# Performance work log

Measured on AMD Instinct MI355X. Metric: run time of the kernel, lower is better.

Reference implementation:

```python
import jax, jax.numpy as jnp
import numpy as np

B, N, C, F = 8, 3, 64, 128
H = W = 128


def _up2(x):
    # nearest-neighbor upsample by 2 on the last two axes
    return jnp.repeat(jnp.repeat(x, 2, axis=-2), 2, axis=-1)


def setup_inputs() -> dict:
    key = jax.random.key(0)
    ks = jax.random.split(key, 12)
    s = lambda k, shp, fan: jax.random.normal(k, shp, jnp.float32) * (1.0 / np.sqrt(fan))
    return {
        "contexts": jax.random.normal(ks[0], (B, N, C, H, W), jnp.float32),
        "mainstream": jax.random.normal(ks[1], (B, F, H // 2, W // 2), jnp.float32),
        "Wc": s(ks[2], (C, C), C),        # W_context 1x1 conv weight [out,in]
        "bc": jnp.zeros((C,), jnp.float32),
        "Wf": s(ks[3], (C, F), F),        # W_feat 1x1
        "bf": jnp.zeros((C,), jnp.float32),
        "Wk": s(ks[4], (C, F), F),        # W_key_feat 1x1
        "bk": jnp.zeros((C,), jnp.float32),
        "Vw": s(ks[5], (C, F, 3, 3), F * 9),  # values_conv 3x3, OIHW
        "Vb": jnp.zeros((C,), jnp.float32),
    }


def reference(contexts, mainstream, Wc, bc, Wf, bf, Wk, bk, Vw, Vb):
    # contexts: [B,N,C,H,W], mainstream: [B,F,h,w]
    bias = lambda b: b[None, :, None, None]
    queries = jnp.einsum('bfhw,cf->bchw', mainstream, Wf) + bias(bf)       # [B,C,h,w]
    keys_m = jnp.einsum('bfhw,cf->bchw', mainstream, Wk) + bias(bk)        # [B,C,h,w]
    values = jax.lax.conv_general_dilated(
        mainstream, Vw, (1, 1), 'SAME',
        dimension_numbers=('NCHW', 'OIHW', 'NCHW')) + bias(Vb)             # [B,C,h,w]

    # stack contexts with upsampled mainstream keys, project with W_context (1x1)
    keys_stack = jnp.concatenate([contexts, _up2(keys_m)[:, None]], axis=1)  # [B,N+1,C,H,W]
    keys_proj = jnp.einsum('bnchw,dc->bndhw', keys_stack, Wc) + bc[None, None, :, None, None]

    q_up = _up2(queries)                                                    # [B,C,H,W]
    logits = jnp.einsum('bnchw,bchw->bnhw', keys_proj, q_up)                # [B,N+1,H,W]
    attn = jax.nn.softmax(logits, axis=1)                                   # softmax over contexts

    vals_stack = jnp.concatenate([contexts, _up2(values)[:, None]], axis=1) # [B,N+1,C,H,W]
    out = jnp.einsum('bnchw,bnhw->bchw', vals_stack, attn)                  # [B,C,H,W]
    return out
```

## Files before the change

kernel.cpp:

```cpp
#include <hip/hip_runtime.h>
#include <math.h>

#define CH   64
#define FD   128
#define HS   64
#define FS   128
#define NB   8
#define NCTX 3

#define WS_QT   0
#define WS_VAL  2097152
#define WS_L3   4194304
#define WS_BQ   4227072
#define WS_AVH  4227136
#define WS_AVL  4264000
#define WS_AQH  4300864
#define WS_AQL  4304960
#define WS_AKH  4309056
#define WS_AKL  4313152
#define WS_MTH  4317248
#define WS_MTL  6547520

typedef short  s16x8  __attribute__((ext_vector_type(8)));
typedef float  f32x16 __attribute__((ext_vector_type(16)));

__device__ inline unsigned short bf16_rne(float x) {
  unsigned u = __float_as_uint(x);
  u += 0x7FFFu + ((u >> 16) & 1u);
  return (unsigned short)(u >> 16);
}
__device__ inline void split2(float x, unsigned short& h, unsigned short& l) {
  h = bf16_rne(x);
  l = bf16_rne(x - __uint_as_float((unsigned)h << 16));
}

__global__ __launch_bounds__(256) void a_prep(
    const float* __restrict__ Wc, const float* __restrict__ Wf,
    const float* __restrict__ bf, const float* __restrict__ Wk,
    const float* __restrict__ Vw, float* __restrict__ ws) {
  int id = blockIdx.x * 256 + threadIdx.x;
  unsigned short* avh = (unsigned short*)(ws + WS_AVH);
  unsigned short* avl = (unsigned short*)(ws + WS_AVL);
  unsigned short* aqh = (unsigned short*)(ws + WS_AQH);
  unsigned short* aql = (unsigned short*)(ws + WS_AQL);
  unsigned short* akh = (unsigned short*)(ws + WS_AKH);
  unsigned short* akl = (unsigned short*)(ws + WS_AKL);

  if (id < 9216) {
    int tile = id / 4608, rem = id % 4608;
    int q = rem >> 6, l = rem & 63;
    int am = l & 31, kh = l >> 5;
    int c = tile * 32 + am, tap = q >> 3, kf = q & 7;
#pragma unroll
    for (int j = 0; j < 8; ++j) {
      int f = kf * 16 + kh * 8 + j;
      unsigned short h, lo;
      split2(Vw[(c * FD + f) * 9 + tap], h, lo);
      avh[id * 8 + j] = h; avl[id * 8 + j] = lo;
    }
  } else if (id < 10240) {
    int i2 = id - 9216;
    int tile = i2 >> 9, rem = i2 & 511;
    int q = rem >> 6, l = rem & 63;
    int am = l & 31, kh = l >> 5;
    int c = tile * 32 + am;
#pragma unroll
    for (int j = 0; j < 8; ++j) {
      int f = q * 16 + kh * 8 + j;
      float acc = 0.f;
      for (int d = 0; d < CH; ++d)
        acc = fmaf(Wc[d * CH + c], Wf[d * FD + f], acc);
      unsigned short h, lo; split2(acc, h, lo);
      aqh[i2 * 8 + j] = h; aql[i2 * 8 + j] = lo;
    }
  } else if (id < 11264) {
    int i3 = id - 10240;
    int tile = i3 >> 9, rem = i3 & 511;
    int q = rem >> 6, l = rem & 63;
    int am = l & 31, kh = l >> 5;
    int c = tile * 32 + am;
#pragma unroll
    for (int j = 0; j < 8; ++j) {
      int f = q * 16 + kh * 8 + j;
      unsigned short h, lo; split2(Wk[c * FD + f], h, lo);
      akh[i3 * 8 + j] = h; akl[i3 * 8 + j] = lo;
    }
  } else if (id < 11328) {
    int c = id - 11264;
    float acc = 0.f;
    for (int d = 0; d < CH; ++d) acc = fmaf(Wc[d * CH + c], bf[d], acc);
    ws[WS_BQ + c] = acc;
  }
}

__global__ __launch_bounds__(256) void m_setup(
    const float* __restrict__ m, unsigned short* __restrict__ mth,
    unsigned short* __restrict__ mtl) {
  const int b = blockIdx.x / 66, yp = blockIdx.x % 66;
  const int lane = threadIdx.x & 63;
  const int wave = threadIdx.x >> 6;
  const int yy = yp - 1;
  const bool rowok = (yy >= 0) && (yy < HS);
#pragma unroll
  for (int cc = 0; cc < 4; ++cc) {
    const int f0 = wave * 32 + cc * 8;
    float v[8];
    if (rowok) {
#pragma unroll
      for (int j = 0; j < 8; ++j)
        v[j] = m[((b * FD + f0 + j) * HS + yy) * HS + lane];
    } else {
#pragma unroll
      for (int j = 0; j < 8; ++j) v[j] = 0.f;
    }
    s16x8 hi, lo;
#pragma unroll
    for (int j = 0; j < 8; ++j) {
      unsigned short h, l; split2(v[j], h, l);
      hi[j] = (short)h; lo[j] = (short)l;
    }
    size_t base = ((size_t)(b * 66 + yp) * 66 + (lane + 1)) * FD + f0;
    *(s16x8*)(mth + base) = hi;
    *(s16x8*)(mtl + base) = lo;
    if (lane < 2) {
      s16x8 z;
#pragma unroll
      for (int j = 0; j < 8; ++j) z[j] = 0;
      size_t bb = ((size_t)(b * 66 + yp) * 66 + lane * 65) * FD + f0;
      *(s16x8*)(mth + bb) = z;
      *(s16x8*)(mtl + bb) = z;
    }
  }
}

__global__ __launch_bounds__(512) void main_mfma(
    const unsigned short* __restrict__ mth, const unsigned short* __restrict__ mtl,
    const float* __restrict__ Vb, const float* __restrict__ bk,
    float* __restrict__ ws) {
  const int b = blockIdx.x >> 6, y = blockIdx.x & 63;
  const int t = threadIdx.x, lane = t & 63;
  const int wave = __builtin_amdgcn_readfirstlane(t >> 6);
  const int am = lane & 31, kh = lane >> 5;
  const int w4 = wave & 3;
  const int x0 = (w4 & 1) * 32, ch0 = (w4 >> 1) * 32;
  const int ct = w4 >> 1;
  const int khalf = wave >> 2;

  const unsigned short* avh = (const unsigned short*)(ws + WS_AVH);
  const unsigned short* avl = (const unsigned short*)(ws + WS_AVL);

  __shared__ float red[4][16][64];
  __shared__ float qtb[2][64][32];
  __shared__ float keb[2][64][32];

  f32x16 a1, a2;
#pragma unroll
  for (int i = 0; i < 16; ++i) { a1[i] = 0.f; a2[i] = 0.f; }
#pragma unroll 4
  for (int qi = 0; qi < 36; ++qi) {
    const int q = khalf * 36 + qi;
    const int tap = q >> 3, kf = q & 7;
    const s16x8 ah = *(const s16x8*)(avh + ((ct * 72 + q) * 64 + lane) * 8);
    const s16x8 al = *(const s16x8*)(avl + ((ct * 72 + q) * 64 + lane) * 8);
    const int row = y + tap / 3;
    const int col = x0 + am + tap % 3;
    const s16x8 bh = *(const s16x8*)(mth +
        ((size_t)(b * 66 + row) * 66 + col) * FD + kf * 16 + kh * 8);
    a1 = __builtin_amdgcn_mfma_f32_32x32x16_bf16(ah, bh, a1, 0, 0, 0);
    a2 = __builtin_amdgcn_mfma_f32_32x32x16_bf16(al, bh, a2, 0, 0, 0);
  }
  if (khalf) {
#pragma unroll
    for (int r = 0; r < 16; ++r) red[w4][r][lane] = a1[r] + a2[r];
  }
  __syncthreads();
  if (!khalf) {
#pragma unroll
    for (int r = 0; r < 16; ++r) {
      const int c = ch0 + (r & 3) + 8 * (r >> 2) + 4 * kh;
      float v = a1[r] + a2[r] + red[w4][r][lane] + Vb[c];
      ws[WS_VAL + ((b * CH + c) * HS + y) * HS + x0 + am] = v;
    }
  }

  const unsigned short* Ah = (const unsigned short*)(ws + (khalf ? WS_AKH : WS_AQH));
  const unsigned short* Al = (const unsigned short*)(ws + (khalf ? WS_AKL : WS_AQL));
  f32x16 c1, c2;
#pragma unroll
  for (int i = 0; i < 16; ++i) { c1[i] = 0.f; c2[i] = 0.f; }
#pragma unroll
  for (int q = 0; q < 8; ++q) {
    const s16x8 ah = *(const s16x8*)(Ah + ((ct * 8 + q) * 64 + lane) * 8);
    const s16x8 al = *(const s16x8*)(Al + ((ct * 8 + q) * 64 + lane) * 8);
    const size_t base = ((size_t)(b * 66 + y + 1) * 66 + (x0 + am + 1)) * FD
                        + q * 16 + kh * 8;
    const s16x8 bh = *(const s16x8*)(mth + base);
    const s16x8 bl = *(const s16x8*)(mtl + base);
    c1 = __builtin_amdgcn_mfma_f32_32x32x16_bf16(ah, bh, c1, 0, 0, 0);
    c1 = __builtin_amdgcn_mfma_f32_32x32x16_bf16(al, bh, c1, 0, 0, 0);
    c2 = __builtin_amdgcn_mfma_f32_32x32x16_bf16(ah, bl, c2, 0, 0, 0);
  }
  const int ptile = w4 & 1;
#pragma unroll
  for (int r = 0; r < 16; ++r) {
    const int c = ch0 + (r & 3) + 8 * (r >> 2) + 4 * kh;
    if (khalf) {
      keb[ptile][c][am] = c1[r] + c2[r] + bk[c];
    } else {
      float v = c1[r] + c2[r] + ws[WS_BQ + c];
      qtb[ptile][c][am] = v;
      ws[WS_QT + ((b * CH + c) * HS + y) * HS + x0 + am] = v;
    }
  }
  __syncthreads();

  if (wave < 2) {
    float s = 0.f;
#pragma unroll 8
    for (int j = 0; j < 32; ++j)
      s = fmaf(qtb[wave][kh * 32 + j][am], keb[wave][kh * 32 + j][am], s);
    s += __shfl_xor(s, 32, 64);
    if (kh == 0)
      ws[WS_L3 + (b * HS + y) * HS + wave * 32 + am] = s;
  }
}

__global__ __launch_bounds__(256) void fullres_kernel(
    const float* __restrict__ ctx, const float* __restrict__ ws,
    float* __restrict__ out) {
  const int xh = blockIdx.x & 1, hrow = blockIdx.x >> 1;
  const int b = blockIdx.y;
  const int px = threadIdx.x & 63, cg = threadIdx.x >> 6;
  const int x = xh * 64 + px;
  const int h2 = hrow >> 1, w2 = x >> 1;

  const float* qtp = ws + WS_QT + (size_t)(b * CH) * HS * HS + h2 * HS + w2;
  const float* cb  = ctx + (size_t)(b * NCTX * CH) * FS * FS + hrow * FS + x;
  const int cs = FS * FS, ns = CH * FS * FS;

  float l0 = 0.f, l1 = 0.f, l2 = 0.f;
#pragma unroll
  for (int j = 0; j < 16; ++j) {
    const int c = cg * 16 + j;
    const float q = qtp[c * HS * HS];
    l0 = fmaf(cb[c * cs], q, l0);
    l1 = fmaf(cb[ns + c * cs], q, l1);
    l2 = fmaf(cb[2 * ns + c * cs], q, l2);
  }
  __shared__ float red[3][4][64];
  red[0][cg][px] = l0; red[1][cg][px] = l1; red[2][cg][px] = l2;
  __syncthreads();
  float L0 = red[0][0][px] + red[0][1][px] + red[0][2][px] + red[0][3][px];
  float L1 = red[1][0][px] + red[1][1][px] + red[1][2][px] + red[1][3][px];
  float L2 = red[2][0][px] + red[2][1][px] + red[2][2][px] + red[2][3][px];
  float L3 = ws[WS_L3 + (b * HS + h2) * HS + w2];

  float mx = fmaxf(fmaxf(L0, L1), fmaxf(L2, L3));
  float e0 = __expf(L0 - mx), e1 = __expf(L1 - mx);
  float e2 = __expf(L2 - mx), e3 = __expf(L3 - mx);
  float inv = 1.f / (e0 + e1 + e2 + e3);
  float a0 = e0 * inv, a1 = e1 * inv, a2 = e2 * inv, a3 = e3 * inv;

  const float* valp = ws + WS_VAL + (size_t)(b * CH) * HS * HS + h2 * HS + w2;
  float* op = out + (size_t)(b * CH) * FS * FS + hrow * FS + x;
#pragma unroll
  for (int j = 0; j < 16; ++j) {
    const int c = cg * 16 + j;
    float o = a3 * valp[c * HS * HS];
    o = fmaf(a0, cb[c * cs], o);
    o = fmaf(a1, cb[ns + c * cs], o);
    o = fmaf(a2, cb[2 * ns + c * cs], o);
    op[c * cs] = o;
  }
}

extern "C" void kernel_launch(void* const* d_in, const int* in_sizes, int n_in,
                              void* d_out, int out_size, void* d_ws, size_t ws_size,
                              hipStream_t stream) {
  const float* ctx = (const float*)d_in[0];
  const float* ms  = (const float*)d_in[1];
  const float* Wc  = (const float*)d_in[2];
  const float* Wf  = (const float*)d_in[4];
  const float* bf  = (const float*)d_in[5];
  const float* Wk  = (const float*)d_in[6];
  const float* bk  = (const float*)d_in[7];
  const float* Vw  = (const float*)d_in[8];
  const float* Vb  = (const float*)d_in[9];
  float* ws  = (float*)d_ws;
  float* out = (float*)d_out;

  unsigned short* mth = (unsigned short*)(ws + WS_MTH);
  unsigned short* mtl = (unsigned short*)(ws + WS_MTL);

  a_prep<<<45, 256, 0, stream>>>(Wc, Wf, bf, Wk, Vw, ws);
  m_setup<<<NB * 66, 256, 0, stream>>>(ms, mth, mtl);
  main_mfma<<<NB * HS, 512, 0, stream>>>(mth, mtl, Vb, bk, ws);
  fullres_kernel<<<dim3(2 * FS, NB), 256, 0, stream>>>(ctx, ws, out);
}
```

Baseline: 292.2 us.

## Fuse setup kernels, relayout mainstream tile by k-chunk, cache context reads in registers

Merges the weight-prep and mainstream-split kernels into one launch, removing one kernel launch. Changes the padded bf16 mainstream layout to [b][row][kf][col][kh][8], so the 32 lanes of an MFMA B-fragment load read contiguous 16-byte chunks instead of chunks spaced a full 256-byte row apart. In the full-res kernel, the three context values per channel are kept in registers and reused in the output pass instead of being reloaded from global memory, which raises register pressure.

```diff
diff --git a/kernel.cpp b/kernel.cpp
--- a/kernel.cpp
+++ b/kernel.cpp
@@ -21,6 +21,9 @@
 #define WS_MTH  4317248
 #define WS_MTL  6547520
 
+#define MT2_IDX(b,row,kf,col,kh) \
+  ((((((size_t)(b)*66+(row))*8+(kf))*66+(col))*2+(kh))*8)
+
 typedef short  s16x8  __attribute__((ext_vector_type(8)));
 typedef float  f32x16 __attribute__((ext_vector_type(16)));
 
@@ -34,101 +37,104 @@
   l = bf16_rne(x - __uint_as_float((unsigned)h << 16));
 }
 
-__global__ __launch_bounds__(256) void a_prep(
+__global__ __launch_bounds__(256) void setup_all(
     const float* __restrict__ Wc, const float* __restrict__ Wf,
     const float* __restrict__ bf, const float* __restrict__ Wk,
-    const float* __restrict__ Vw, float* __restrict__ ws) {
-  int id = blockIdx.x * 256 + threadIdx.x;
-  unsigned short* avh = (unsigned short*)(ws + WS_AVH);
-  unsigned short* avl = (unsigned short*)(ws + WS_AVL);
-  unsigned short* aqh = (unsigned short*)(ws + WS_AQH);
-  unsigned short* aql = (unsigned short*)(ws + WS_AQL);
-  unsigned short* akh = (unsigned short*)(ws + WS_AKH);
-  unsigned short* akl = (unsigned short*)(ws + WS_AKL);
-
-  if (id < 9216) {
-    int tile = id / 4608, rem = id % 4608;
-    int q = rem >> 6, l = rem & 63;
-    int am = l & 31, kh = l >> 5;
-    int c = tile * 32 + am, tap = q >> 3, kf = q & 7;
-#pragma unroll
-    for (int j = 0; j < 8; ++j) {
-      int f = kf * 16 + kh * 8 + j;
-      unsigned short h, lo;
-      split2(Vw[(c * FD + f) * 9 + tap], h, lo);
-      avh[id * 8 + j] = h; avl[id * 8 + j] = lo;
+    const float* __restrict__ Vw, const float* __restrict__ m,
+    float* __restrict__ ws) {
+  if (blockIdx.x < 45) {
+    int id = blockIdx.x * 256 + threadIdx.x;
+    unsigned short* avh = (unsigned short*)(ws + WS_AVH);
+    unsigned short* avl = (unsigned short*)(ws + WS_AVL);
+    unsigned short* aqh = (unsigned short*)(ws + WS_AQH);
+    unsigned short* aql = (unsigned short*)(ws + WS_AQL);
+    unsigned short* akh = (unsigned short*)(ws + WS_AKH);
+    unsigned short* akl = (unsigned short*)(ws + WS_AKL);
+
+    if (id < 9216) {
+      int tile = id / 4608, rem = id % 4608;
+      int q = rem >> 6, l = rem & 63;
+      int am = l & 31, kh = l >> 5;
+      int c = tile * 32 + am, tap = q >> 3, kf = q & 7;
+#pragma unroll
+      for (int j = 0; j < 8; ++j) {
+        int f = kf * 16 + kh * 8 + j;
+        unsigned short h, lo;
+        split2(Vw[(c * FD + f) * 9 + tap], h, lo);
+        avh[id * 8 + j] = h; avl[id * 8 + j] = lo;
+      }
+    } else if (id < 10240) {
+      int i2 = id - 9216;
+      int tile = i2 >> 9, rem = i2 & 511;
+      int q = rem >> 6, l = rem & 63;
+      int am = l & 31, kh = l >> 5;
+      int c = tile * 32 + am;
+#pragma unroll
+      for (int j = 0; j < 8; ++j) {
+        int f = q * 16 + kh * 8 + j;
+        float acc = 0.f;
+        for (int d = 0; d < CH; ++d)
+          acc = fmaf(Wc[d * CH + c], Wf[d * FD + f], acc);
+        unsigned short h, lo; split2(acc, h, lo);
+        aqh[i2 * 8 + j] = h; aql[i2 * 8 + j] = lo;
+      }
+    } else if (id < 11264) {
+      int i3 = id - 10240;
+      int tile = i3 >> 9, rem = i3 & 511;
+      int q = rem >> 6, l = rem & 63;
+      int am = l & 31, kh = l >> 5;
+      int c = tile * 32 + am;
+#pragma unroll
+      for (int j = 0; j < 8; ++j) {
+        int f = q * 16 + kh * 8 + j;
+        unsigned short h, lo; split2(Wk[c * FD + f], h, lo);
+        akh[i3 * 8 + j] = h; akl[i3 * 8 + j] = lo;
+      }
+    } else if (id < 11328) {
+      int c = id - 11264;
+      float acc = 0.f;
+      for (int d = 0; d < CH; ++d) acc = fmaf(Wc[d * CH + c], bf[d], acc);
+      ws[WS_BQ + c] = acc;
     }
-  } else if (id < 10240) {
-    int i2 = id - 9216;
-    int tile = i2 >> 9, rem = i2 & 511;
-    int q = rem >> 6, l = rem & 63;
-    int am = l & 31, kh = l >> 5;
-    int c = tile * 32 + am;
-#pragma unroll
-    for (int j = 0; j < 8; ++j) {
-      int f = q * 16 + kh * 8 + j;
-      float acc = 0.f;
-      for (int d = 0; d < CH; ++d)
-        acc = fmaf(Wc[d * CH + c], Wf[d * FD + f], acc);
-      unsigned short h, lo; split2(acc, h, lo);
-      aqh[i2 * 8 + j] = h; aql[i2 * 8 + j] = lo;
-    }
-  } else if (id < 11264) {
-    int i3 = id - 10240;
-    int tile = i3 >> 9, rem = i3 & 511;
-    int q = rem >> 6, l = rem & 63;
-    int am = l & 31, kh = l >> 5;
-    int c = tile * 32 + am;
-#pragma unroll
-    for (int j = 0; j < 8; ++j) {
-      int f = q * 16 + kh * 8 + j;
-      unsigned short h, lo; split2(Wk[c * FD + f], h, lo);
-      akh[i3 * 8 + j] = h; akl[i3 * 8 + j] = lo;
-    }
-  } else if (id < 11328) {
-    int c = id - 11264;
-    float acc = 0.f;
-    for (int d = 0; d < CH; ++d) acc = fmaf(Wc[d * CH + c], bf[d], acc);
-    ws[WS_BQ + c] = acc;
-  }
-}
-
-__global__ __launch_bounds__(256) void m_setup(
-    const float* __restrict__ m, unsigned short* __restrict__ mth,
-    unsigned short* __restrict__ mtl) {
-  const int b = blockIdx.x / 66, yp = blockIdx.x % 66;
-  const int lane = threadIdx.x & 63;
-  const int wave = threadIdx.x >> 6;
-  const int yy = yp - 1;
-  const bool rowok = (yy >= 0) && (yy < HS);
-#pragma unroll
-  for (int cc = 0; cc < 4; ++cc) {
-    const int f0 = wave * 32 + cc * 8;
-    float v[8];
-    if (rowok) {
-#pragma unroll
-      for (int j = 0; j < 8; ++j)
-        v[j] = m[((b * FD + f0 + j) * HS + yy) * HS + lane];
-    } else {
-#pragma unroll
-      for (int j = 0; j < 8; ++j) v[j] = 0.f;
-    }
-    s16x8 hi, lo;
-#pragma unroll
-    for (int j = 0; j < 8; ++j) {
-      unsigned short h, l; split2(v[j], h, l);
-      hi[j] = (short)h; lo[j] = (short)l;
-    }
-    size_t base = ((size_t)(b * 66 + yp) * 66 + (lane + 1)) * FD + f0;
-    *(s16x8*)(mth + base) = hi;
-    *(s16x8*)(mtl + base) = lo;
-    if (lane < 2) {
-      s16x8 z;
-#pragma unroll
-      for (int j = 0; j < 8; ++j) z[j] = 0;
-      size_t bb = ((size_t)(b * 66 + yp) * 66 + lane * 65) * FD + f0;
-      *(s16x8*)(mth + bb) = z;
-      *(s16x8*)(mtl + bb) = z;
+  } else {
+    unsigned short* mth = (unsigned short*)(ws + WS_MTH);
+    unsigned short* mtl = (unsigned short*)(ws + WS_MTL);
+    const int bid = blockIdx.x - 45;
+    const int b = bid / 66, yp = bid % 66;
+    const int lane = threadIdx.x & 63;
+    const int wave = threadIdx.x >> 6;
+    const int yy = yp - 1;
+    const bool rowok = (yy >= 0) && (yy < HS);
+#pragma unroll
+    for (int cc = 0; cc < 4; ++cc) {
+      const int f0 = wave * 32 + cc * 8;
+      const int kf = f0 >> 4, kh = (f0 >> 3) & 1;
+      float v[8];
+      if (rowok) {
+#pragma unroll
+        for (int j = 0; j < 8; ++j)
+          v[j] = m[((b * FD + f0 + j) * HS + yy) * HS + lane];
+      } else {
+#pragma unroll
+        for (int j = 0; j < 8; ++j) v[j] = 0.f;
+      }
+      s16x8 hi, lo;
+#pragma unroll
+      for (int j = 0; j < 8; ++j) {
+        unsigned short h, l; split2(v[j], h, l);
+        hi[j] = (short)h; lo[j] = (short)l;
+      }
+      size_t base = MT2_IDX(b, yp, kf, lane + 1, kh);
+      *(s16x8*)(mth + base) = hi;
+      *(s16x8*)(mtl + base) = lo;
+      if (lane < 2) {
+        s16x8 z;
+#pragma unroll
+        for (int j = 0; j < 8; ++j) z[j] = 0;
+        size_t bb = MT2_IDX(b, yp, kf, lane * 65, kh);
+        *(s16x8*)(mth + bb) = z;
+        *(s16x8*)(mtl + bb) = z;
+      }
     }
   }
 }
@@ -162,10 +168,8 @@
     const int tap = q >> 3, kf = q & 7;
     const s16x8 ah = *(const s16x8*)(avh + ((ct * 72 + q) * 64 + lane) * 8);
     const s16x8 al = *(const s16x8*)(avl + ((ct * 72 + q) * 64 + lane) * 8);
-    const int row = y + tap / 3;
-    const int col = x0 + am + tap % 3;
     const s16x8 bh = *(const s16x8*)(mth +
-        ((size_t)(b * 66 + row) * 66 + col) * FD + kf * 16 + kh * 8);
+        MT2_IDX(b, y + tap / 3, kf, x0 + am + tap % 3, kh));
     a1 = __builtin_amdgcn_mfma_f32_32x32x16_bf16(ah, bh, a1, 0, 0, 0);
     a2 = __builtin_amdgcn_mfma_f32_32x32x16_bf16(al, bh, a2, 0, 0, 0);
   }
@@ -192,8 +196,7 @@
   for (int q = 0; q < 8; ++q) {
     const s16x8 ah = *(const s16x8*)(Ah + ((ct * 8 + q) * 64 + lane) * 8);
     const s16x8 al = *(const s16x8*)(Al + ((ct * 8 + q) * 64 + lane) * 8);
-    const size_t base = ((size_t)(b * 66 + y + 1) * 66 + (x0 + am + 1)) * FD
-                        + q * 16 + kh * 8;
+    const size_t base = MT2_IDX(b, y + 1, q, x0 + am + 1, kh);
     const s16x8 bh = *(const s16x8*)(mth + base);
     const s16x8 bl = *(const s16x8*)(mtl + base);
     c1 = __builtin_amdgcn_mfma_f32_32x32x16_bf16(ah, bh, c1, 0, 0, 0);
@@ -238,14 +241,18 @@
   const float* cb  = ctx + (size_t)(b * NCTX * CH) * FS * FS + hrow * FS + x;
   const int cs = FS * FS, ns = CH * FS * FS;
 
+  float cv0[16], cv1[16], cv2[16];
   float l0 = 0.f, l1 = 0.f, l2 = 0.f;
 #pragma unroll
   for (int j = 0; j < 16; ++j) {
     const int c = cg * 16 + j;
+    cv0[j] = cb[c * cs];
+    cv1[j] = cb[ns + c * cs];
+    cv2[j] = cb[2 * ns + c * cs];
     const float q = qtp[c * HS * HS];
-    l0 = fmaf(cb[c * cs], q, l0);
-    l1 = fmaf(cb[ns + c * cs], q, l1);
-    l2 = fmaf(cb[2 * ns + c * cs], q, l2);
+    l0 = fmaf(cv0[j], q, l0);
+    l1 = fmaf(cv1[j], q, l1);
+    l2 = fmaf(cv2[j], q, l2);
   }
   __shared__ float red[3][4][64];
   red[0][cg][px] = l0; red[1][cg][px] = l1; red[2][cg][px] = l2;
@@ -267,9 +274,9 @@
   for (int j = 0; j < 16; ++j) {
     const int c = cg * 16 + j;
     float o = a3 * valp[c * HS * HS];
-    o = fmaf(a0, cb[c * cs], o);
-    o = fmaf(a1, cb[ns + c * cs], o);
-    o = fmaf(a2, cb[2 * ns + c * cs], o);
+    o = fmaf(a0, cv0[j], o);
+    o = fmaf(a1, cv1[j], o);
+    o = fmaf(a2, cv2[j], o);
     op[c * cs] = o;
   }
 }
@@ -292,8 +299,7 @@
   unsigned short* mth = (unsigned short*)(ws + WS_MTH);
   unsigned short* mtl = (unsigned short*)(ws + WS_MTL);
 
-  a_prep<<<45, 256, 0, stream>>>(Wc, Wf, bf, Wk, Vw, ws);
-  m_setup<<<NB * 66, 256, 0, stream>>>(ms, mth, mtl);
+  setup_all<<<45 + NB * 66, 256, 0, stream>>>(Wc, Wf, bf, Wk, Vw, ms, ws);
   main_mfma<<<NB * HS, 512, 0, stream>>>(mth, mtl, Vb, bk, ws);
   fullres_kernel<<<dim3(2 * FS, NB), 256, 0, stream>>>(ctx, ws, out);
 }
```

After: 271.3 us. 1.08x faster.
